# Optimization experiments

Measured on AMD Instinct MI355X. Metric: run time of the kernel, lower is better.

Reference implementation:

```python
import jax, jax.numpy as jnp
import numpy as np
from jax import lax

N_WIRES = 4
EPS_BN = 1e-5

def _conv(x, w, b):
    y = lax.conv_general_dilated(x, w, (1, 1), 'SAME',
                                 dimension_numbers=('NCHW', 'OIHW', 'NCHW'))
    return y + b[None, :, None, None]

def _bn2d(x, g, b):
    mu = jnp.mean(x, axis=(0, 2, 3), keepdims=True)
    var = jnp.var(x, axis=(0, 2, 3), keepdims=True)
    return (x - mu) * lax.rsqrt(var + EPS_BN) * g[None, :, None, None] + b[None, :, None, None]

def _maxpool2(x):
    return lax.reduce_window(x, -jnp.inf, lax.max, (1, 1, 2, 2), (1, 1, 2, 2), 'VALID')

def _ry(t):
    c, s = jnp.cos(t / 2), jnp.sin(t / 2)
    return jnp.stack([jnp.stack([c, -s], -1), jnp.stack([s, c], -1)], -2).astype(jnp.complex64)

def _rz(t):
    tc = t.astype(jnp.complex64)
    em, ep = jnp.exp(-0.5j * tc), jnp.exp(0.5j * tc)
    z = jnp.zeros_like(em)
    return jnp.stack([jnpp_stack := jnp.stack([em, z], -1), jnp.stack([z, ep], -1)], -2)

def _rx(t):
    c = jnp.cos(t / 2).astype(jnp.complex64)
    s = (-1j) * jnp.sin(t / 2).astype(jnp.complex64)
    return jnp.stack([jnp.stack([c, s], -1), jnp.stack([s, c], -1)], -2)

def _apply_1q(state, U, q):
    # state: (B,2,2,2,2); U: (2,2) shared or (B,2,2) per-sample
    a = jnp.moveaxis(state, 1 + q, 1)
    if U.ndim == 2:
        a = jnp.einsum('ij,bj...->bi...', U, a)
    else:
        a = jnp.einsum('bij,bj...->bi...', U, a)
    return jnp.moveaxis(a, 1, 1 + q)

def _cnot(state, c, t):
    a = jnp.moveaxis(state, (1 + c, 1 + t), (1, 2))
    a = jnp.stack([a[:, 0], jnp.flip(a[:, 1], axis=1)], axis=1)
    return jnp.moveaxis(a, (1, 2), (1 + c, 1 + t))

def _circuit(scaled, theta, rho):
    # scaled: (B, 4) angles; theta, rho: (4, 3)
    B = scaled.shape[0]
    state = jnp.zeros((B,) + (2,) * N_WIRES, jnp.complex64)
    state = state.at[(slice(None),) + (0,) * N_WIRES].set(1.0 + 0j)
    for i in range(N_WIRES):
        state = _apply_1q(state, _ry(scaled[:, i]), i)
    for i in range(N_WIRES):
        state = _apply_1q(state, _ry(theta[i, 0]), i)
        state = _apply_1q(state, _rz(theta[i, 1]), i)
        state = _apply_1q(state, _rx(theta[i, 2]), i)
    for i in range(N_WIRES - 1):
        state = _cnot(state, i, i + 1)
    for i in range(N_WIRES):
        state = _apply_1q(state, _ry(rho[i, 0]), i)
        state = _apply_1q(state, _rz(rho[i, 1]), i)
        state = _apply_1q(state, _rx(rho[i, 2]), i)
    for i in range(N_WIRES - 1):
        state = _cnot(state, i + 1, i)
    probs = jnp.abs(state) ** 2  # (B,2,2,2,2)
    exps = []
    for i in range(N_WIRES):
        p = jnp.moveaxis(probs, 1 + i, 1)
        exps.append(jnp.sum(p[:, 0], axis=(1, 2, 3)) - jnp.sum(p[:, 1], axis=(1, 2, 3)))
    return jnp.stack(exps, axis=1)  # (B,4)

def setup_inputs() -> dict:
    key = jax.random.key(0)
    ks = jax.random.split(key, 8)
    B = 128
    return {
        'x': jax.random.normal(ks[0], (B, 1, 224, 224), jnp.float32),
        'conv1_w': jax.random.normal(ks[1], (8, 1, 3, 3), jnp.float32) * 0.1,
        'conv1_b': jnp.zeros((8,), jnp.float32),
        'bn1_g': jnp.ones((8,), jnp.float32),
        'bn1_b': jnp.zeros((8,), jnp.float32),
        'conv2_w': jax.random.normal(ks[2], (16, 8, 3, 3), jnp.float32) * 0.1,
        'conv2_b': jnp.zeros((16,), jnp.float32),
        'bn2_g': jnp.ones((16,), jnp.float32),
        'bn2_b': jnp.zeros((16,), jnp.float32),
        'theta': jax.random.normal(ks[3], (4, 3), jnp.float32),
        'rho': jax.random.normal(ks[4], (4, 3), jnp.float32),
        'norm_g': jnp.ones((4,), jnp.float32),
        'norm_b': jnp.zeros((4,), jnp.float32),
    }

def reference(x, conv1_w, conv1_b, bn1_g, bn1_b, conv2_w, conv2_b, bn2_g, bn2_b,
              theta, rho, norm_g, norm_b):
    h = jax.nn.relu(_bn2d(_conv(x, conv1_w, conv1_b), bn1_g, bn1_b))
    h = _maxpool2(h)
    h = jax.nn.relu(_bn2d(_conv(h, conv2_w, conv2_b), bn2_g, bn2_b))
    h = _maxpool2(h)
    feat = jnp.mean(h, axis=(2, 3))          # AdaptiveAvgPool2d((1,1)) + flatten -> (B,16)
    feat = feat[:, :N_WIRES]                  # (B,4)
    scaled = (feat - jnp.mean(feat)) / (jnp.std(feat, ddof=1) + 1e-6) * jnp.pi
    out = _circuit(scaled, theta, rho)        # (B,4) real
    mu = jnp.mean(out, axis=0, keepdims=True)
    var = jnp.var(out, axis=0, keepdims=True)
    return (out - mu) * lax.rsqrt(var + EPS_BN) * norm_g[None, :] + norm_b[None, :]
```

## Files before the change

kernel.cpp:

```cpp
#include <hip/hip_runtime.h>
#include <math.h>

#define H1 224
#define W1 224
#define H2 112
#define W2 112
#define HP 56
#define WP 56

#define NS 32
#define SLOT_STRIDE 64

struct C2 { float re, im; };
__device__ __forceinline__ C2 cmul(C2 a, C2 b) {
    return C2{fmaf(a.re, b.re, -a.im * b.im), fmaf(a.re, b.im, a.im * b.re)};
}
__device__ __forceinline__ C2 cadd(C2 a, C2 b) { return C2{a.re + b.re, a.im + b.im}; }

template <int S>
__device__ __forceinline__ void ap1s(C2* st, C2 u00, C2 u01, C2 u10, C2 u11) {
#pragma unroll
    for (int i = 0; i < 16; i++) {
        if (i & S) continue;
        C2 a0 = st[i], a1 = st[i + S];
        st[i]     = cadd(cmul(u00, a0), cmul(u01, a1));
        st[i + S] = cadd(cmul(u10, a0), cmul(u11, a1));
    }
}

template <int SC, int STT>
__device__ __forceinline__ void cnot_s(C2* st) {
#pragma unroll
    for (int i = 0; i < 16; i++)
        if ((i & SC) && !(i & STT)) { C2 t = st[i]; st[i] = st[i + STT]; st[i + STT] = t; }
}

struct M2 { C2 m[2][2]; };
__device__ __forceinline__ M2 mmul(const M2& A, const M2& B) {
    M2 R;
#pragma unroll
    for (int i = 0; i < 2; i++)
#pragma unroll
        for (int j = 0; j < 2; j++)
            R.m[i][j] = cadd(cmul(A.m[i][0], B.m[0][j]), cmul(A.m[i][1], B.m[1][j]));
    return R;
}

__device__ __forceinline__ M2 combined_u(const float* __restrict__ p) {
    float c0 = cosf(0.5f * p[0]), s0 = sinf(0.5f * p[0]);
    float c1 = cosf(0.5f * p[1]), s1 = sinf(0.5f * p[1]);
    float c2 = cosf(0.5f * p[2]), s2 = sinf(0.5f * p[2]);
    M2 Ry = {{{{c0, 0.f}, {-s0, 0.f}}, {{s0, 0.f}, {c0, 0.f}}}};
    M2 Rz = {{{{c1, -s1}, {0.f, 0.f}}, {{0.f, 0.f}, {c1, s1}}}};
    M2 Rx = {{{{c2, 0.f}, {0.f, -s2}}, {{0.f, -s2}, {c2, 0.f}}}};
    return mmul(Rx, mmul(Rz, Ry));
}

template <int Q>
__device__ __forceinline__ void rows_reduce(float* red, const float* vals, int tid) {
#pragma unroll
    for (int q = 0; q < Q; q++) red[q * 256 + tid] = vals[q];
    __syncthreads();
    for (int s = 128; s > 0; s >>= 1) {
        for (int idx = tid; idx < Q * s; idx += 256) {
            int row = idx / s, i = idx - row * s;
            red[row * 256 + i] += red[row * 256 + i + s];
        }
        __syncthreads();
    }
}

__global__ void zero_ws(float* ws, int n) {
    int i = blockIdx.x * blockDim.x + threadIdx.x;
    if (i < n) ws[i] = 0.f;
}

__global__ void conv1_stats(const float* __restrict__ x, const float* __restrict__ w,
                            const float* __restrict__ bias, float* __restrict__ stats) {
    __shared__ float red[16 * 256];
    int strip = blockIdx.x;
    int b = blockIdx.y;
    int tid = threadIdx.x;
    const float* xb = x + (size_t)b * H1 * W1;
    float sums[8], sqs[8];
#pragma unroll
    for (int c = 0; c < 8; c++) { sums[c] = 0.f; sqs[c] = 0.f; }
    int col = tid;
    if (col < W1) {
        bool cl = col > 0, cr = col < W1 - 1;
        int row0 = strip * 32;
        float a0, a1, a2, b0, b1, b2, c0, c1, c2;
        {
            int r = row0 - 1;
            if (r >= 0) {
                a0 = cl ? xb[r * W1 + col - 1] : 0.f;
                a1 = xb[r * W1 + col];
                a2 = cr ? xb[r * W1 + col + 1] : 0.f;
            } else { a0 = a1 = a2 = 0.f; }
            r = row0;
            b0 = cl ? xb[r * W1 + col - 1] : 0.f;
            b1 = xb[r * W1 + col];
            b2 = cr ? xb[r * W1 + col + 1] : 0.f;
        }
        for (int rr = 0; rr < 32; rr++) {
            int rn = row0 + rr + 1;
            if (rn < H1) {
                c0 = cl ? xb[rn * W1 + col - 1] : 0.f;
                c1 = xb[rn * W1 + col];
                c2 = cr ? xb[rn * W1 + col + 1] : 0.f;
            } else { c0 = c1 = c2 = 0.f; }
#pragma unroll
            for (int c = 0; c < 8; c++) {
                float acc = bias[c];
                acc = fmaf(w[c * 9 + 0], a0, acc);
                acc = fmaf(w[c * 9 + 1], a1, acc);
                acc = fmaf(w[c * 9 + 2], a2, acc);
                acc = fmaf(w[c * 9 + 3], b0, acc);
                acc = fmaf(w[c * 9 + 4], b1, acc);
                acc = fmaf(w[c * 9 + 5], b2, acc);
                acc = fmaf(w[c * 9 + 6], c0, acc);
                acc = fmaf(w[c * 9 + 7], c1, acc);
                acc = fmaf(w[c * 9 + 8], c2, acc);
                sums[c] += acc;
                sqs[c] = fmaf(acc, acc, sqs[c]);
            }
            a0 = b0; a1 = b1; a2 = b2;
            b0 = c0; b1 = c1; b2 = c2;
        }
    }
    float vals[16];
#pragma unroll
    for (int c = 0; c < 8; c++) { vals[c] = sums[c]; vals[8 + c] = sqs[c]; }
    rows_reduce<16>(red, vals, tid);
    int slot = (b * 7 + strip) & (NS - 1);
    if (tid < 16) atomicAdd(stats + slot * SLOT_STRIDE + tid, red[tid * 256]);
}

__device__ __forceinline__ float slot_sum(const float* stats, int c) {
    float s = 0.f;
#pragma unroll
    for (int sl = 0; sl < NS; sl++) s += stats[sl * SLOT_STRIDE + c];
    return s;
}

template <int PH, int PW>
__device__ __forceinline__ void build_h1_tile(const float* __restrict__ xb,
                                              float (*h1t)[PH][PW],
                                              const float* __restrict__ w1,
                                              const float* __restrict__ b1,
                                              const float* sc1, const float* sh1,
                                              int oy0, int ox0, int tid) {
    for (int i = tid; i < PH * PW; i += 256) {
        int p = i / PW, q = i % PW;
        int hy = oy0 + p, hx = ox0 + q;
        bool ok = (hy >= 0 && hy < H2 && hx >= 0 && hx < W2);
        float xp[5][5];
        if (hy >= 1 && hy <= H2 - 2 && hx >= 1 && hx <= W2 - 2) {
            const float* bp = xb + (2 * hy - 1) * W1 + (2 * hx - 1);
#pragma unroll
            for (int r = 0; r < 5; r++)
#pragma unroll
                for (int c = 0; c < 5; c++) xp[r][c] = bp[r * W1 + c];
        } else if (ok) {
#pragma unroll
            for (int r = 0; r < 5; r++)
#pragma unroll
                for (int c = 0; c < 5; c++) {
                    int gy = 2 * hy - 1 + r, gx = 2 * hx - 1 + c;
                    xp[r][c] = (gy >= 0 && gy < H1 && gx >= 0 && gx < W1) ? xb[gy * W1 + gx] : 0.f;
                }
        }
#pragma unroll
        for (int c = 0; c < 8; c++) {
            float mx = 0.f;
            if (ok) {
                mx = -INFINITY;
#pragma unroll
                for (int dy = 0; dy < 2; dy++)
#pragma unroll
                    for (int dx = 0; dx < 2; dx++) {
                        float acc = b1[c];
#pragma unroll
                        for (int ky = 0; ky < 3; ky++)
#pragma unroll
                            for (int kx = 0; kx < 3; kx++)
                                acc = fmaf(w1[c * 9 + ky * 3 + kx], xp[dy + ky][dx + kx], acc);
                        mx = fmaxf(mx, fmaxf(fmaf(acc, sc1[c], sh1[c]), 0.f));
                    }
            }
            h1t[c][p][q] = mx;
        }
    }
}

template <bool STORE>
__global__ __launch_bounds__(256, 4) void conv2_stats_fused(
        const float* __restrict__ x, const float* __restrict__ w1,
        const float* __restrict__ b1, const float* __restrict__ g1,
        const float* __restrict__ be1, const float* __restrict__ stats1,
        const float* __restrict__ w2, const float* __restrict__ b2,
        float* __restrict__ stats2,
        float* __restrict__ pmax, float* __restrict__ pmin, float N1) {
    __shared__ __align__(16) float h1t[8][34][34];
    __shared__ float sc1[8], sh1[8];
    int b = blockIdx.z;
    int Y0 = blockIdx.y * 32, X0 = blockIdx.x * 32;
    int ty = threadIdx.y, tx = threadIdx.x;
    int tid = ty * 16 + tx;
    if (tid < 8) {
        float su = slot_sum(stats1, tid), sq = slot_sum(stats1, 8 + tid);
        float mu = su / N1;
        float var = sq / N1 - mu * mu;
        float sc = g1[tid] * rsqrtf(var + 1e-5f);
        sc1[tid] = sc;
        sh1[tid] = be1[tid] - mu * sc;
    }
    __syncthreads();
    const float* xb = x + (size_t)b * H1 * W1;
    build_h1_tile<34, 34>(xb, h1t, w1, b1, sc1, sh1, Y0 - 1, X0 - 1, tid);
    __syncthreads();
    float acc[4][2][2];
#pragma unroll
    for (int co = 0; co < 4; co++)
#pragma unroll
        for (int dy = 0; dy < 2; dy++)
#pragma unroll
            for (int dx = 0; dx < 2; dx++) acc[co][dy][dx] = b2[co];
#pragma unroll
    for (int ci = 0; ci < 8; ci++) {
        float win[4][4];
#pragma unroll
        for (int r = 0; r < 4; r++) {
            const float2* rp = (const float2*)&h1t[ci][2 * ty + r][2 * tx];
            float2 u = rp[0], v = rp[1];
            win[r][0] = u.x; win[r][1] = u.y; win[r][2] = v.x; win[r][3] = v.y;
        }
#pragma unroll
        for (int co = 0; co < 4; co++)
#pragma unroll
            for (int ky = 0; ky < 3; ky++)
#pragma unroll
                for (int kx = 0; kx < 3; kx++) {
                    float wv = w2[co * 72 + ci * 9 + ky * 3 + kx];
#pragma unroll
                    for (int dy = 0; dy < 2; dy++)
#pragma unroll
                        for (int dx = 0; dx < 2; dx++)
                            acc[co][dy][dx] = fmaf(wv, win[dy + ky][dx + kx], acc[co][dy][dx]);
                }
    }
    int cy0 = Y0 + 2 * ty, cx0 = X0 + 2 * tx;
    bool vy0 = cy0 < H2, vy1 = cy0 + 1 < H2, vx0 = cx0 < W2, vx1 = cx0 + 1 < W2;
    float vals[8];
#pragma unroll
    for (int co = 0; co < 4; co++) {
        float s = 0.f, q = 0.f;
        if (vy0 && vx0) { float a = acc[co][0][0]; s += a; q = fmaf(a, a, q); }
        if (vy0 && vx1) { float a = acc[co][0][1]; s += a; q = fmaf(a, a, q); }
        if (vy1 && vx0) { float a = acc[co][1][0]; s += a; q = fmaf(a, a, q); }
        if (vy1 && vx1) { float a = acc[co][1][1]; s += a; q = fmaf(a, a, q); }
        vals[co] = s;
        vals[4 + co] = q;
    }
    if (STORE) {
        int hy = (Y0 >> 1) + ty, hx = (X0 >> 1) + tx;
        if (hy < HP && hx < WP) {
#pragma unroll
            for (int co = 0; co < 4; co++) {
                float mx = fmaxf(fmaxf(acc[co][0][0], acc[co][0][1]),
                                 fmaxf(acc[co][1][0], acc[co][1][1]));
                float mn = fminf(fminf(acc[co][0][0], acc[co][0][1]),
                                 fminf(acc[co][1][0], acc[co][1][1]));
                size_t idx = (((size_t)b * 4 + co) * HP + hy) * WP + hx;
                pmax[idx] = mx;
                pmin[idx] = mn;
            }
        }
    }
    __syncthreads();
    float* red = (float*)h1t;
    rows_reduce<8>(red, vals, tid);
    int slot = ((b * 16) + blockIdx.y * 4 + blockIdx.x) & (NS - 1);
    if (tid < 8) atomicAdd(stats2 + slot * SLOT_STRIDE + tid, red[tid * 256]);
}

__global__ void pool_bn_mean(const float* __restrict__ pmax, const float* __restrict__ pmin,
                             const float* __restrict__ g2, const float* __restrict__ be2,
                             const float* __restrict__ stats2,
                             float* __restrict__ featbuf, float N2) {
    __shared__ float red[256];
    int co = blockIdx.x & 3;
    int b = blockIdx.x >> 2;
    int tid = threadIdx.x;
    float su = slot_sum(stats2, co), sq = slot_sum(stats2, 4 + co);
    float mu = su / N2;
    float var = sq / N2 - mu * mu;
    float sc = g2[co] * rsqrtf(var + 1e-5f);
    float sh = be2[co] - mu * sc;
    const float* P = (sc >= 0.f ? pmax : pmin) + ((size_t)b * 4 + co) * (HP * WP);
    float s = 0.f;
    for (int i = tid; i < HP * WP; i += 256) s += fmaxf(fmaf(P[i], sc, sh), 0.f);
    red[tid] = s;
    __syncthreads();
    for (int st = 128; st > 0; st >>= 1) {
        if (tid < st) red[tid] += red[tid + st];
        __syncthreads();
    }
    if (tid == 0) featbuf[(size_t)b * 4 + co] = red[0];
}

__global__ void conv2_final_fused(const float* __restrict__ x, const float* __restrict__ w1,
                                  const float* __restrict__ b1, const float* __restrict__ g1,
                                  const float* __restrict__ be1,
                                  const float* __restrict__ stats1,
                                  const float* __restrict__ w2, const float* __restrict__ b2,
                                  const float* __restrict__ g2, const float* __restrict__ be2,
                                  const float* __restrict__ stats2,
                                  float* __restrict__ featbuf, float N1, float N2) {
    __shared__ __align__(16) float h1t[8][34][34];
    __shared__ float sc1[8], sh1[8];
    __shared__ float sc2[4], sh2[4];
    int b = blockIdx.z;
    int py0 = blockIdx.y * 16, px0 = blockIdx.x * 16;
    int ty = threadIdx.y, tx = threadIdx.x;
    int tid = ty * 16 + tx;
    if (tid < 8) {
        float su = slot_sum(stats1, tid), sq = slot_sum(stats1, 8 + tid);
        float mu = su / N1;
        float var = sq / N1 - mu * mu;
        float sc = g1[tid] * rsqrtf(var + 1e-5f);
        sc1[tid] = sc;
        sh1[tid] = be1[tid] - mu * sc;
    }
    if (tid >= 16 && tid < 20) {
        int j = tid - 16;
        float su = slot_sum(stats2, j), sq = slot_sum(stats2, 4 + j);
        float mu = su / N2;
        float var = sq / N2 - mu * mu;
        float sc = g2[j] * rsqrtf(var + 1e-5f);
        sc2[j] = sc;
        sh2[j] = be2[j] - mu * sc;
    }
    __syncthreads();
    const float* xb = x + (size_t)b * H1 * W1;
    build_h1_tile<34, 34>(xb, h1t, w1, b1, sc1, sh1, 2 * py0 - 1, 2 * px0 - 1, tid);
    __syncthreads();
    bool valid = (py0 + ty < HP) && (px0 + tx < WP);
    float acc[4][2][2];
#pragma unroll
    for (int co = 0; co < 4; co++)
#pragma unroll
        for (int dy = 0; dy < 2; dy++)
#pragma unroll
            for (int dx = 0; dx < 2; dx++) acc[co][dy][dx] = b2[co];
#pragma unroll
    for (int ci = 0; ci < 8; ci++) {
        float win[4][4];
#pragma unroll
        for (int r = 0; r < 4; r++) {
            const float2* rp = (const float2*)&h1t[ci][2 * ty + r][2 * tx];
            float2 u = rp[0], v = rp[1];
            win[r][0] = u.x; win[r][1] = u.y; win[r][2] = v.x; win[r][3] = v.y;
        }
#pragma unroll
        for (int co = 0; co < 4; co++)
#pragma unroll
            for (int ky = 0; ky < 3; ky++)
#pragma unroll
                for (int kx = 0; kx < 3; kx++) {
                    float wv = w2[co * 72 + ci * 9 + ky * 3 + kx];
#pragma unroll
                    for (int dy = 0; dy < 2; dy++)
#pragma unroll
                        for (int dx = 0; dx < 2; dx++)
                            acc[co][dy][dx] = fmaf(wv, win[dy + ky][dx + kx], acc[co][dy][dx]);
                }
    }
    float vals[4];
#pragma unroll
    for (int co = 0; co < 4; co++) {
        float mx = -INFINITY;
#pragma unroll
        for (int dy = 0; dy < 2; dy++)
#pragma unroll
            for (int dx = 0; dx < 2; dx++)
                mx = fmaxf(mx, fmaxf(fmaf(acc[co][dy][dx], sc2[co], sh2[co]), 0.f));
        vals[co] = valid ? mx : 0.f;
    }
    __syncthreads();
    float* red = (float*)h1t;
    rows_reduce<4>(red, vals, tid);
    if (tid < 4) atomicAdd(featbuf + (size_t)b * 4 + tid, red[tid * 256]);
}

__device__ __forceinline__ float bsum(float v, float* lds) {
#pragma unroll
    for (int off = 32; off; off >>= 1) v += __shfl_xor(v, off, 64);
    __syncthreads();
    if ((threadIdx.x & 63) == 0) lds[threadIdx.x >> 6] = v;
    __syncthreads();
    float r = 0.f;
    int nw = (int)(blockDim.x + 63) >> 6;
#pragma clang loop unroll(disable)
    for (int i = 0; i < nw; i++) r += lds[i];
    return r;
}

__global__ void finalize(const float* __restrict__ featbuf, const float* __restrict__ theta,
                         const float* __restrict__ rho, const float* __restrict__ ng,
                         const float* __restrict__ nb, float* __restrict__ out, int B) {
    __shared__ float lds[16];
    int b = threadIdx.x;
    float f[4];
#pragma unroll
    for (int j = 0; j < 4; j++) f[j] = featbuf[b * 4 + j] * (1.f / (HP * WP));

    float n = 4.f * (float)B;
    float mean = bsum(f[0] + f[1] + f[2] + f[3], lds) / n;
    float d2 = 0.f;
#pragma unroll
    for (int j = 0; j < 4; j++) { float d = f[j] - mean; d2 += d * d; }
    float var1 = bsum(d2, lds) / (n - 1.f);
    float stdv = sqrtf(fmaxf(var1, 0.f)) + 1e-6f;
    const float PI = 3.14159265358979323846f;
    float cs[4], sn[4];
#pragma unroll
    for (int j = 0; j < 4; j++) {
        float sc = (f[j] - mean) / stdv * PI;
        cs[j] = cosf(0.5f * sc);
        sn[j] = sinf(0.5f * sc);
    }

    C2 st[16];
    {
        float amp[16];
        amp[0] = 1.f;
        amp[1] = sn[3]; amp[0] = cs[3];
#pragma unroll
        for (int k = 0; k < 2; k++) { amp[k + 2] = amp[k] * sn[2]; amp[k] *= cs[2]; }
#pragma unroll
        for (int k = 0; k < 4; k++) { amp[k + 4] = amp[k] * sn[1]; amp[k] *= cs[1]; }
#pragma unroll
        for (int k = 0; k < 8; k++) { amp[k + 8] = amp[k] * sn[0]; amp[k] *= cs[0]; }
#pragma unroll
        for (int i = 0; i < 16; i++) st[i] = C2{amp[i], 0.f};
    }

#pragma clang loop unroll(disable)
    for (int l = 0; l < 2; l++) {
        const float* p = (l == 0) ? theta : rho;
#pragma clang loop unroll(disable)
        for (int i = 0; i < 4; i++) {
            M2 U = combined_u(p + i * 3);
            switch (i) {
            case 0: ap1s<8>(st, U.m[0][0], U.m[0][1], U.m[1][0], U.m[1][1]); break;
            case 1: ap1s<4>(st, U.m[0][0], U.m[0][1], U.m[1][0], U.m[1][1]); break;
            case 2: ap1s<2>(st, U.m[0][0], U.m[0][1], U.m[1][0], U.m[1][1]); break;
            default: ap1s<1>(st, U.m[0][0], U.m[0][1], U.m[1][0], U.m[1][1]); break;
            }
        }
        if (l == 0) { cnot_s<8, 4>(st); cnot_s<4, 2>(st); cnot_s<2, 1>(st); }
        else        { cnot_s<4, 8>(st); cnot_s<2, 4>(st); cnot_s<1, 2>(st); }
    }

    float e[4];
#pragma unroll
    for (int qb = 0; qb < 4; qb++) {
        int m = 8 >> qb;
        float p0 = 0.f, p1 = 0.f;
#pragma unroll
        for (int i = 0; i < 16; i++) {
            float pr = st[i].re * st[i].re + st[i].im * st[i].im;
            if (i & m) p1 += pr; else p0 += pr;
        }
        e[qb] = p0 - p1;
    }

#pragma clang loop unroll(disable)
    for (int j = 0; j < 4; j++) {
        float mu = bsum(e[j], lds) / (float)B;
        float dv = e[j] - mu;
        float v = bsum(dv * dv, lds) / (float)B;
        out[b * 4 + j] = fmaf(dv, rsqrtf(v + 1e-5f) * ng[j], nb[j]);
    }
}

extern "C" void kernel_launch(void* const* d_in, const int* in_sizes, int n_in,
                              void* d_out, int out_size, void* d_ws, size_t ws_size,
                              hipStream_t stream) {
    const float* x     = (const float*)d_in[0];
    const float* w1    = (const float*)d_in[1];
    const float* b1    = (const float*)d_in[2];
    const float* g1    = (const float*)d_in[3];
    const float* be1   = (const float*)d_in[4];
    const float* w2    = (const float*)d_in[5];
    const float* b2    = (const float*)d_in[6];
    const float* g2    = (const float*)d_in[7];
    const float* be2   = (const float*)d_in[8];
    const float* theta = (const float*)d_in[9];
    const float* rho   = (const float*)d_in[10];
    const float* ng    = (const float*)d_in[11];
    const float* nb    = (const float*)d_in[12];
    float* out = (float*)d_out;

    int B = in_sizes[0] / (H1 * W1);

    float* ws = (float*)d_ws;
    float* stats1 = ws;
    float* stats2 = ws + NS * SLOT_STRIDE;
    float* featbuf = ws + 2 * NS * SLOT_STRIDE;
    float* pmax = featbuf + (size_t)B * 4;
    float* pmin = pmax + (size_t)B * 4 * HP * WP;

    size_t need_store = ((size_t)2 * NS * SLOT_STRIDE + (size_t)B * 4 +
                         (size_t)2 * B * 4 * HP * WP) * sizeof(float);
    bool store = ws_size >= need_store;

    float N1 = (float)B * H1 * W1;
    float N2 = (float)B * H2 * W2;
    int nz = 2 * NS * SLOT_STRIDE + B * 4;

    zero_ws<<<(nz + 255) / 256, 256, 0, stream>>>(ws, nz);
    conv1_stats<<<dim3(7, B), 256, 0, stream>>>(x, w1, b1, stats1);
    if (store) {
        conv2_stats_fused<true><<<dim3(4, 4, B), dim3(16, 16), 0, stream>>>(
            x, w1, b1, g1, be1, stats1, w2, b2, stats2, pmax, pmin, N1);
        pool_bn_mean<<<B * 4, 256, 0, stream>>>(pmax, pmin, g2, be2, stats2, featbuf, N2);
    } else {
        conv2_stats_fused<false><<<dim3(4, 4, B), dim3(16, 16), 0, stream>>>(
            x, w1, b1, g1, be1, stats1, w2, b2, stats2, nullptr, nullptr, N1);
        conv2_final_fused<<<dim3(4, 4, B), dim3(16, 16), 0, stream>>>(
            x, w1, b1, g1, be1, stats1, w2, b2, g2, be2, stats2, featbuf, N1, N2);
    }
    finalize<<<1, B, 0, stream>>>(featbuf, theta, rho, ng, nb, out, B);
}
```

Baseline: 191.6 us.

## Store pooled conv1 pre-BN output and slim conv2 to avoid recomputing conv1

Conv1 now also writes a 2x2 max- or min-pooled pre-BN map, picking max or min by the sign of the BN gamma so pooling can come before the affine BN and ReLU. Conv2 then reads this 112x112 buffer instead of recomputing conv1 from x. It stores only the sign-selected pooled value, which halves the pool2 buffer. The final stage is split into a per-sample circuit kernel plus a BN kernel that use atomic global sums, replacing the single-block finalize. This trades extra workspace traffic and more launches for removing the redundant conv1 work.

```diff
diff --git a/kernel.cpp b/kernel.cpp
--- a/kernel.cpp
+++ b/kernel.cpp
@@ -27,14 +27,12 @@
         st[i + S] = cadd(cmul(u10, a0), cmul(u11, a1));
     }
 }
-
 template <int SC, int STT>
 __device__ __forceinline__ void cnot_s(C2* st) {
 #pragma unroll
     for (int i = 0; i < 16; i++)
         if ((i & SC) && !(i & STT)) { C2 t = st[i]; st[i] = st[i + STT]; st[i + STT] = t; }
 }
-
 struct M2 { C2 m[2][2]; };
 __device__ __forceinline__ M2 mmul(const M2& A, const M2& B) {
     M2 R;
@@ -45,7 +43,6 @@
             R.m[i][j] = cadd(cmul(A.m[i][0], B.m[0][j]), cmul(A.m[i][1], B.m[1][j]));
     return R;
 }
-
 __device__ __forceinline__ M2 combined_u(const float* __restrict__ p) {
     float c0 = cosf(0.5f * p[0]), s0 = sinf(0.5f * p[0]);
     float c1 = cosf(0.5f * p[1]), s1 = sinf(0.5f * p[1]);
@@ -73,6 +70,87 @@
 __global__ void zero_ws(float* ws, int n) {
     int i = blockIdx.x * blockDim.x + threadIdx.x;
     if (i < n) ws[i] = 0.f;
+}
+
+__device__ __forceinline__ float slot_sum(const float* stats, int c) {
+    float s = 0.f;
+#pragma unroll
+    for (int sl = 0; sl < NS; sl++) s += stats[sl * SLOT_STRIDE + c];
+    return s;
+}
+
+__global__ void conv1_pool_stats(const float* __restrict__ x, const float* __restrict__ w,
+                                 const float* __restrict__ bias, const float* __restrict__ g1,
+                                 float* __restrict__ stats, float* __restrict__ p1ext) {
+    __shared__ float red[16 * 256];
+    int strip = blockIdx.x;
+    int b = blockIdx.y;
+    int tid = threadIdx.x;
+    const float* xb = x + (size_t)b * H1 * W1;
+    float sums[8], sqs[8], pm[8];
+    bool gp[8];
+#pragma unroll
+    for (int c = 0; c < 8; c++) { sums[c] = 0.f; sqs[c] = 0.f; gp[c] = g1[c] >= 0.f; }
+    int col = tid;
+    if (col < W1) {
+        bool cl = col > 0, cr = col < W1 - 1;
+        int row0 = strip * 32;
+        float a0, a1, a2, b0, b1, b2, c0, c1, c2;
+        {
+            int r = row0 - 1;
+            if (r >= 0) {
+                a0 = cl ? xb[r * W1 + col - 1] : 0.f;
+                a1 = xb[r * W1 + col];
+                a2 = cr ? xb[r * W1 + col + 1] : 0.f;
+            } else { a0 = a1 = a2 = 0.f; }
+            r = row0;
+            b0 = cl ? xb[r * W1 + col - 1] : 0.f;
+            b1 = xb[r * W1 + col];
+            b2 = cr ? xb[r * W1 + col + 1] : 0.f;
+        }
+        for (int rr = 0; rr < 32; rr++) {
+            int rn = row0 + rr + 1;
+            if (rn < H1) {
+                c0 = cl ? xb[rn * W1 + col - 1] : 0.f;
+                c1 = xb[rn * W1 + col];
+                c2 = cr ? xb[rn * W1 + col + 1] : 0.f;
+            } else { c0 = c1 = c2 = 0.f; }
+#pragma unroll
+            for (int c = 0; c < 8; c++) {
+                float acc = bias[c];
+                acc = fmaf(w[c * 9 + 0], a0, acc);
+                acc = fmaf(w[c * 9 + 1], a1, acc);
+                acc = fmaf(w[c * 9 + 2], a2, acc);
+                acc = fmaf(w[c * 9 + 3], b0, acc);
+                acc = fmaf(w[c * 9 + 4], b1, acc);
+                acc = fmaf(w[c * 9 + 5], b2, acc);
+                acc = fmaf(w[c * 9 + 6], c0, acc);
+                acc = fmaf(w[c * 9 + 7], c1, acc);
+                acc = fmaf(w[c * 9 + 8], c2, acc);
+                sums[c] += acc;
+                sqs[c] = fmaf(acc, acc, sqs[c]);
+                if ((rr & 1) == 0) {
+                    pm[c] = acc;
+                } else {
+                    float m = gp[c] ? fmaxf(pm[c], acc) : fminf(pm[c], acc);
+                    float mo = __shfl_xor(m, 1, 64);
+                    m = gp[c] ? fmaxf(m, mo) : fminf(m, mo);
+                    if ((tid & 1) == 0) {
+                        int prow = strip * 16 + (rr >> 1);
+                        p1ext[(((size_t)b * 8 + c) * H2 + prow) * W2 + (col >> 1)] = m;
+                    }
+                }
+            }
+            a0 = b0; a1 = b1; a2 = b2;
+            b0 = c0; b1 = c1; b2 = c2;
+        }
+    }
+    float vals[16];
+#pragma unroll
+    for (int c = 0; c < 8; c++) { vals[c] = sums[c]; vals[8 + c] = sqs[c]; }
+    rows_reduce<16>(red, vals, tid);
+    int slot = (b * 7 + strip) & (NS - 1);
+    if (tid < 16) atomicAdd(stats + slot * SLOT_STRIDE + tid, red[tid * 256]);
 }
 
 __global__ void conv1_stats(const float* __restrict__ x, const float* __restrict__ w,
@@ -136,13 +214,6 @@
     if (tid < 16) atomicAdd(stats + slot * SLOT_STRIDE + tid, red[tid * 256]);
 }
 
-__device__ __forceinline__ float slot_sum(const float* stats, int c) {
-    float s = 0.f;
-#pragma unroll
-    for (int sl = 0; sl < NS; sl++) s += stats[sl * SLOT_STRIDE + c];
-    return s;
-}
-
 template <int PH, int PW>
 __device__ __forceinline__ void build_h1_tile(const float* __restrict__ xb,
                                               float (*h1t)[PH][PW],
@@ -191,6 +262,99 @@
             h1t[c][p][q] = mx;
         }
     }
+}
+
+__global__ __launch_bounds__(256, 4) void conv2_stats_slim(
+        const float* __restrict__ p1ext, const float* __restrict__ g1,
+        const float* __restrict__ be1, const float* __restrict__ stats1,
+        const float* __restrict__ w2, const float* __restrict__ b2,
+        const float* __restrict__ g2,
+        float* __restrict__ stats2, float* __restrict__ p2ext, float N1) {
+    __shared__ __align__(16) float h1t[8][30][30];
+    __shared__ float sc1[8], sh1[8];
+    int b = blockIdx.z;
+    int Y0 = blockIdx.y * 28, X0 = blockIdx.x * 28;
+    int ty = threadIdx.y, tx = threadIdx.x;
+    int tid = ty * 16 + tx;
+    if (tid < 8) {
+        float su = slot_sum(stats1, tid), sq = slot_sum(stats1, 8 + tid);
+        float mu = su / N1;
+        float var = sq / N1 - mu * mu;
+        float sc = g1[tid] * rsqrtf(var + 1e-5f);
+        sc1[tid] = sc;
+        sh1[tid] = be1[tid] - mu * sc;
+    }
+    __syncthreads();
+    const float* pb = p1ext + (size_t)b * 8 * H2 * W2;
+    for (int i = tid; i < 8 * 30 * 30; i += 256) {
+        int c = i / 900, r = (i % 900) / 30, q = i % 30;
+        int hy = Y0 - 1 + r, hx = X0 - 1 + q;
+        float v = 0.f;
+        if (hy >= 0 && hy < H2 && hx >= 0 && hx < W2) {
+            float e = pb[c * H2 * W2 + hy * W2 + hx];
+            v = fmaxf(fmaf(e, sc1[c], sh1[c]), 0.f);
+        }
+        h1t[c][r][q] = v;
+    }
+    __syncthreads();
+    bool act = (ty < 14) && (tx < 14);
+    float acc[4][2][2];
+#pragma unroll
+    for (int co = 0; co < 4; co++)
+#pragma unroll
+        for (int dy = 0; dy < 2; dy++)
+#pragma unroll
+            for (int dx = 0; dx < 2; dx++) acc[co][dy][dx] = b2[co];
+    if (act) {
+#pragma unroll
+        for (int ci = 0; ci < 8; ci++) {
+            float win[4][4];
+#pragma unroll
+            for (int r = 0; r < 4; r++) {
+                const float2* rp = (const float2*)&h1t[ci][2 * ty + r][2 * tx];
+                float2 u = rp[0], v = rp[1];
+                win[r][0] = u.x; win[r][1] = u.y; win[r][2] = v.x; win[r][3] = v.y;
+            }
+#pragma unroll
+            for (int co = 0; co < 4; co++)
+#pragma unroll
+                for (int ky = 0; ky < 3; ky++)
+#pragma unroll
+                    for (int kx = 0; kx < 3; kx++) {
+                        float wv = w2[co * 72 + ci * 9 + ky * 3 + kx];
+#pragma unroll
+                        for (int dy = 0; dy < 2; dy++)
+#pragma unroll
+                            for (int dx = 0; dx < 2; dx++)
+                                acc[co][dy][dx] = fmaf(wv, win[dy + ky][dx + kx], acc[co][dy][dx]);
+                    }
+        }
+    }
+    float vals[8];
+#pragma unroll
+    for (int co = 0; co < 4; co++) {
+        float s = acc[co][0][0] + acc[co][0][1] + acc[co][1][0] + acc[co][1][1];
+        float q = acc[co][0][0] * acc[co][0][0] + acc[co][0][1] * acc[co][0][1] +
+                  acc[co][1][0] * acc[co][1][0] + acc[co][1][1] * acc[co][1][1];
+        vals[co] = act ? s : 0.f;
+        vals[4 + co] = act ? q : 0.f;
+    }
+    if (act) {
+        int hy = (Y0 >> 1) + ty, hx = (X0 >> 1) + tx;
+#pragma unroll
+        for (int co = 0; co < 4; co++) {
+            float mx = fmaxf(fmaxf(acc[co][0][0], acc[co][0][1]),
+                             fmaxf(acc[co][1][0], acc[co][1][1]));
+            float mn = fminf(fminf(acc[co][0][0], acc[co][0][1]),
+                             fminf(acc[co][1][0], acc[co][1][1]));
+            p2ext[(((size_t)b * 4 + co) * HP + hy) * WP + hx] = (g2[co] >= 0.f) ? mx : mn;
+        }
+    }
+    __syncthreads();
+    float* red = (float*)h1t;
+    rows_reduce<8>(red, vals, tid);
+    int slot = ((b * 16) + blockIdx.y * 4 + blockIdx.x) & (NS - 1);
+    if (tid < 8) atomicAdd(stats2 + slot * SLOT_STRIDE + tid, red[tid * 256]);
 }
 
 template <bool STORE>
@@ -287,7 +451,7 @@
 __global__ void pool_bn_mean(const float* __restrict__ pmax, const float* __restrict__ pmin,
                              const float* __restrict__ g2, const float* __restrict__ be2,
                              const float* __restrict__ stats2,
-                             float* __restrict__ featbuf, float N2) {
+                             float* __restrict__ featbuf, float* __restrict__ gstats, float N2) {
     __shared__ float red[256];
     int co = blockIdx.x & 3;
     int b = blockIdx.x >> 2;
@@ -306,7 +470,12 @@
         if (tid < st) red[tid] += red[tid + st];
         __syncthreads();
     }
-    if (tid == 0) featbuf[(size_t)b * 4 + co] = red[0];
+    if (tid == 0) {
+        featbuf[(size_t)b * 4 + co] = red[0];
+        float f = red[0] * (1.f / (HP * WP));
+        atomicAdd(gstats + 0, f);
+        atomicAdd(gstats + 1, f * f);
+    }
 }
 
 __global__ void conv2_final_fused(const float* __restrict__ x, const float* __restrict__ w1,
@@ -393,34 +562,16 @@
     if (tid < 4) atomicAdd(featbuf + (size_t)b * 4 + tid, red[tid * 256]);
 }
 
-__device__ __forceinline__ float bsum(float v, float* lds) {
-#pragma unroll
-    for (int off = 32; off; off >>= 1) v += __shfl_xor(v, off, 64);
-    __syncthreads();
-    if ((threadIdx.x & 63) == 0) lds[threadIdx.x >> 6] = v;
-    __syncthreads();
-    float r = 0.f;
-    int nw = (int)(blockDim.x + 63) >> 6;
-#pragma clang loop unroll(disable)
-    for (int i = 0; i < nw; i++) r += lds[i];
-    return r;
-}
-
-__global__ void finalize(const float* __restrict__ featbuf, const float* __restrict__ theta,
-                         const float* __restrict__ rho, const float* __restrict__ ng,
-                         const float* __restrict__ nb, float* __restrict__ out, int B) {
-    __shared__ float lds[16];
-    int b = threadIdx.x;
+__global__ void circuit(const float* __restrict__ featbuf, const float* __restrict__ gstats,
+                        const float* __restrict__ theta, const float* __restrict__ rho,
+                        float* __restrict__ ebuf, float* __restrict__ gst_out, int B) {
+    int b = blockIdx.x;
     float f[4];
 #pragma unroll
     for (int j = 0; j < 4; j++) f[j] = featbuf[b * 4 + j] * (1.f / (HP * WP));
-
     float n = 4.f * (float)B;
-    float mean = bsum(f[0] + f[1] + f[2] + f[3], lds) / n;
-    float d2 = 0.f;
-#pragma unroll
-    for (int j = 0; j < 4; j++) { float d = f[j] - mean; d2 += d * d; }
-    float var1 = bsum(d2, lds) / (n - 1.f);
+    float mean = gstats[0] / n;
+    float var1 = (gstats[1] - n * mean * mean) / (n - 1.f);
     float stdv = sqrtf(fmaxf(var1, 0.f)) + 1e-6f;
     const float PI = 3.14159265358979323846f;
     float cs[4], sn[4];
@@ -430,11 +581,9 @@
         cs[j] = cosf(0.5f * sc);
         sn[j] = sinf(0.5f * sc);
     }
-
     C2 st[16];
     {
         float amp[16];
-        amp[0] = 1.f;
         amp[1] = sn[3]; amp[0] = cs[3];
 #pragma unroll
         for (int k = 0; k < 2; k++) { amp[k + 2] = amp[k] * sn[2]; amp[k] *= cs[2]; }
@@ -445,7 +594,6 @@
 #pragma unroll
         for (int i = 0; i < 16; i++) st[i] = C2{amp[i], 0.f};
     }
-
 #pragma clang loop unroll(disable)
     for (int l = 0; l < 2; l++) {
         const float* p = (l == 0) ? theta : rho;
@@ -462,7 +610,102 @@
         if (l == 0) { cnot_s<8, 4>(st); cnot_s<4, 2>(st); cnot_s<2, 1>(st); }
         else        { cnot_s<4, 8>(st); cnot_s<2, 4>(st); cnot_s<1, 2>(st); }
     }
-
+    if (threadIdx.x == 0) {
+#pragma unroll
+        for (int qb = 0; qb < 4; qb++) {
+            int m = 8 >> qb;
+            float p0 = 0.f, p1 = 0.f;
+#pragma unroll
+            for (int i = 0; i < 16; i++) {
+                float pr = st[i].re * st[i].re + st[i].im * st[i].im;
+                if (i & m) p1 += pr; else p0 += pr;
+            }
+            float e = p0 - p1;
+            ebuf[(size_t)b * 4 + qb] = e;
+            atomicAdd(gst_out + 8 + qb, e);
+            atomicAdd(gst_out + 12 + qb, e * e);
+        }
+    }
+}
+
+__global__ void bn_out(const float* __restrict__ ebuf, const float* __restrict__ gstats,
+                       const float* __restrict__ ng, const float* __restrict__ nb,
+                       float* __restrict__ out, int B) {
+    int b = threadIdx.x;
+#pragma clang loop unroll(disable)
+    for (int j = 0; j < 4; j++) {
+        float mu = gstats[8 + j] / (float)B;
+        float v = gstats[12 + j] / (float)B - mu * mu;
+        float e = ebuf[(size_t)b * 4 + j];
+        out[b * 4 + j] = fmaf(e - mu, rsqrtf(fmaxf(v, 0.f) + 1e-5f) * ng[j], nb[j]);
+    }
+}
+
+__device__ __forceinline__ float bsum(float v, float* lds) {
+#pragma unroll
+    for (int off = 32; off; off >>= 1) v += __shfl_xor(v, off, 64);
+    __syncthreads();
+    if ((threadIdx.x & 63) == 0) lds[threadIdx.x >> 6] = v;
+    __syncthreads();
+    float r = 0.f;
+    int nw = (int)(blockDim.x + 63) >> 6;
+#pragma clang loop unroll(disable)
+    for (int i = 0; i < nw; i++) r += lds[i];
+    return r;
+}
+
+__global__ void finalize(const float* __restrict__ featbuf, const float* __restrict__ theta,
+                         const float* __restrict__ rho, const float* __restrict__ ng,
+                         const float* __restrict__ nb, float* __restrict__ out, int B) {
+    __shared__ float lds[16];
+    int b = threadIdx.x;
+    float f[4];
+#pragma unroll
+    for (int j = 0; j < 4; j++) f[j] = featbuf[b * 4 + j] * (1.f / (HP * WP));
+    float n = 4.f * (float)B;
+    float mean = bsum(f[0] + f[1] + f[2] + f[3], lds) / n;
+    float d2 = 0.f;
+#pragma unroll
+    for (int j = 0; j < 4; j++) { float d = f[j] - mean; d2 += d * d; }
+    float var1 = bsum(d2, lds) / (n - 1.f);
+    float stdv = sqrtf(fmaxf(var1, 0.f)) + 1e-6f;
+    const float PI = 3.14159265358979323846f;
+    float cs[4], sn[4];
+#pragma unroll
+    for (int j = 0; j < 4; j++) {
+        float sc = (f[j] - mean) / stdv * PI;
+        cs[j] = cosf(0.5f * sc);
+        sn[j] = sinf(0.5f * sc);
+    }
+    C2 st[16];
+    {
+        float amp[16];
+        amp[1] = sn[3]; amp[0] = cs[3];
+#pragma unroll
+        for (int k = 0; k < 2; k++) { amp[k + 2] = amp[k] * sn[2]; amp[k] *= cs[2]; }
+#pragma unroll
+        for (int k = 0; k < 4; k++) { amp[k + 4] = amp[k] * sn[1]; amp[k] *= cs[1]; }
+#pragma unroll
+        for (int k = 0; k < 8; k++) { amp[k + 8] = amp[k] * sn[0]; amp[k] *= cs[0]; }
+#pragma unroll
+        for (int i = 0; i < 16; i++) st[i] = C2{amp[i], 0.f};
+    }
+#pragma clang loop unroll(disable)
+    for (int l = 0; l < 2; l++) {
+        const float* p = (l == 0) ? theta : rho;
+#pragma clang loop unroll(disable)
+        for (int i = 0; i < 4; i++) {
+            M2 U = combined_u(p + i * 3);
+            switch (i) {
+            case 0: ap1s<8>(st, U.m[0][0], U.m[0][1], U.m[1][0], U.m[1][1]); break;
+            case 1: ap1s<4>(st, U.m[0][0], U.m[0][1], U.m[1][0], U.m[1][1]); break;
+            case 2: ap1s<2>(st, U.m[0][0], U.m[0][1], U.m[1][0], U.m[1][1]); break;
+            default: ap1s<1>(st, U.m[0][0], U.m[0][1], U.m[1][0], U.m[1][1]); break;
+            }
+        }
+        if (l == 0) { cnot_s<8, 4>(st); cnot_s<4, 2>(st); cnot_s<2, 1>(st); }
+        else        { cnot_s<4, 8>(st); cnot_s<2, 4>(st); cnot_s<1, 2>(st); }
+    }
     float e[4];
 #pragma unroll
     for (int qb = 0; qb < 4; qb++) {
@@ -475,7 +718,6 @@
         }
         e[qb] = p0 - p1;
     }
-
 #pragma clang loop unroll(disable)
     for (int j = 0; j < 4; j++) {
         float mu = bsum(e[j], lds) / (float)B;
@@ -508,29 +750,48 @@
     float* ws = (float*)d_ws;
     float* stats1 = ws;
     float* stats2 = ws + NS * SLOT_STRIDE;
-    float* featbuf = ws + 2 * NS * SLOT_STRIDE;
-    float* pmax = featbuf + (size_t)B * 4;
-    float* pmin = pmax + (size_t)B * 4 * HP * WP;
-
-    size_t need_store = ((size_t)2 * NS * SLOT_STRIDE + (size_t)B * 4 +
-                         (size_t)2 * B * 4 * HP * WP) * sizeof(float);
-    bool store = ws_size >= need_store;
+    float* gstats = ws + 2 * NS * SLOT_STRIDE;
+    float* featbuf = gstats + 64;
+    float* ebuf = featbuf + (size_t)B * 4;
+    float* bufs = ebuf + (size_t)B * 4;
+
+    size_t common = (size_t)(2 * NS * SLOT_STRIDE + 64) + (size_t)B * 8;
+    size_t p2n = (size_t)B * 4 * HP * WP;
+    size_t p1n = (size_t)B * 8 * H2 * W2;
+    size_t needA = (common + p2n + p1n) * sizeof(float);
+    size_t needB = (common + 2 * p2n) * sizeof(float);
+    bool tierA = ws_size >= needA;
+    bool tierB = !tierA && ws_size >= needB;
 
     float N1 = (float)B * H1 * W1;
     float N2 = (float)B * H2 * W2;
-    int nz = 2 * NS * SLOT_STRIDE + B * 4;
+    int nz = (int)common;
 
     zero_ws<<<(nz + 255) / 256, 256, 0, stream>>>(ws, nz);
-    conv1_stats<<<dim3(7, B), 256, 0, stream>>>(x, w1, b1, stats1);
-    if (store) {
+    if (tierA) {
+        float* p2ext = bufs;
+        float* p1ext = bufs + p2n;
+        conv1_pool_stats<<<dim3(7, B), 256, 0, stream>>>(x, w1, b1, g1, stats1, p1ext);
+        conv2_stats_slim<<<dim3(4, 4, B), dim3(16, 16), 0, stream>>>(
+            p1ext, g1, be1, stats1, w2, b2, g2, stats2, p2ext, N1);
+        pool_bn_mean<<<B * 4, 256, 0, stream>>>(p2ext, p2ext, g2, be2, stats2, featbuf, gstats, N2);
+        circuit<<<B, 64, 0, stream>>>(featbuf, gstats, theta, rho, ebuf, gstats, B);
+        bn_out<<<1, B, 0, stream>>>(ebuf, gstats, ng, nb, out, B);
+    } else if (tierB) {
+        float* pmax = bufs;
+        float* pmin = bufs + p2n;
+        conv1_stats<<<dim3(7, B), 256, 0, stream>>>(x, w1, b1, stats1);
         conv2_stats_fused<true><<<dim3(4, 4, B), dim3(16, 16), 0, stream>>>(
             x, w1, b1, g1, be1, stats1, w2, b2, stats2, pmax, pmin, N1);
-        pool_bn_mean<<<B * 4, 256, 0, stream>>>(pmax, pmin, g2, be2, stats2, featbuf, N2);
+        pool_bn_mean<<<B * 4, 256, 0, stream>>>(pmax, pmin, g2, be2, stats2, featbuf, gstats, N2);
+        circuit<<<B, 64, 0, stream>>>(featbuf, gstats, theta, rho, ebuf, gstats, B);
+        bn_out<<<1, B, 0, stream>>>(ebuf, gstats, ng, nb, out, B);
     } else {
+        conv1_stats<<<dim3(7, B), 256, 0, stream>>>(x, w1, b1, stats1);
         conv2_stats_fused<false><<<dim3(4, 4, B), dim3(16, 16), 0, stream>>>(
             x, w1, b1, g1, be1, stats1, w2, b2, stats2, nullptr, nullptr, N1);
         conv2_final_fused<<<dim3(4, 4, B), dim3(16, 16), 0, stream>>>(
             x, w1, b1, g1, be1, stats1, w2, b2, g2, be2, stats2, featbuf, N1, N2);
-    }
-    finalize<<<1, B, 0, stream>>>(featbuf, theta, rho, ng, nb, out, B);
-}
+        finalize<<<1, B, 0, stream>>>(featbuf, theta, rho, ng, nb, out, B);
+    }
+}
```

Measured after the change: 229.9 us. 1.2x slower.

## Split quantum finalize into per-sample circuit blocks and halve conv1 strip height

Applied to the files above, without the earlier changes.

The conv1 statistics pass now uses 16-row strips, which doubles the grid so more workgroups run at once. The single-block finalize is replaced in the stored path by three pieces. pool_bn_mean atomically accumulates the global feature sum and sum of squares. A circuit kernel then runs one block per sample and atomically accumulates the expectation statistics, and a small bn_out kernel applies the final normalization. This is meant to remove the serial single-block circuit evaluation and its block-wide reductions. In exchange it adds a launch, replaces two-pass variance with E[x²]−μ², which can lose precision, and introduces float atomics with nondeterministic summation order.

```diff
diff --git a/kernel.cpp b/kernel.cpp
--- a/kernel.cpp
+++ b/kernel.cpp
@@ -27,14 +27,12 @@
         st[i + S] = cadd(cmul(u10, a0), cmul(u11, a1));
     }
 }
-
 template <int SC, int STT>
 __device__ __forceinline__ void cnot_s(C2* st) {
 #pragma unroll
     for (int i = 0; i < 16; i++)
         if ((i & SC) && !(i & STT)) { C2 t = st[i]; st[i] = st[i + STT]; st[i + STT] = t; }
 }
-
 struct M2 { C2 m[2][2]; };
 __device__ __forceinline__ M2 mmul(const M2& A, const M2& B) {
     M2 R;
@@ -45,7 +43,6 @@
             R.m[i][j] = cadd(cmul(A.m[i][0], B.m[0][j]), cmul(A.m[i][1], B.m[1][j]));
     return R;
 }
-
 __device__ __forceinline__ M2 combined_u(const float* __restrict__ p) {
     float c0 = cosf(0.5f * p[0]), s0 = sinf(0.5f * p[0]);
     float c1 = cosf(0.5f * p[1]), s1 = sinf(0.5f * p[1]);
@@ -61,6 +58,7 @@
 #pragma unroll
     for (int q = 0; q < Q; q++) red[q * 256 + tid] = vals[q];
     __syncthreads();
+#pragma unroll
     for (int s = 128; s > 0; s >>= 1) {
         for (int idx = tid; idx < Q * s; idx += 256) {
             int row = idx / s, i = idx - row * s;
@@ -73,6 +71,13 @@
 __global__ void zero_ws(float* ws, int n) {
     int i = blockIdx.x * blockDim.x + threadIdx.x;
     if (i < n) ws[i] = 0.f;
+}
+
+__device__ __forceinline__ float slot_sum(const float* stats, int c) {
+    float s = 0.f;
+#pragma unroll
+    for (int sl = 0; sl < NS; sl++) s += stats[sl * SLOT_STRIDE + c];
+    return s;
 }
 
 __global__ void conv1_stats(const float* __restrict__ x, const float* __restrict__ w,
@@ -88,7 +93,7 @@
     int col = tid;
     if (col < W1) {
         bool cl = col > 0, cr = col < W1 - 1;
-        int row0 = strip * 32;
+        int row0 = strip * 16;
         float a0, a1, a2, b0, b1, b2, c0, c1, c2;
         {
             int r = row0 - 1;
@@ -102,7 +107,7 @@
             b1 = xb[r * W1 + col];
             b2 = cr ? xb[r * W1 + col + 1] : 0.f;
         }
-        for (int rr = 0; rr < 32; rr++) {
+        for (int rr = 0; rr < 16; rr++) {
             int rn = row0 + rr + 1;
             if (rn < H1) {
                 c0 = cl ? xb[rn * W1 + col - 1] : 0.f;
@@ -132,15 +137,8 @@
 #pragma unroll
     for (int c = 0; c < 8; c++) { vals[c] = sums[c]; vals[8 + c] = sqs[c]; }
     rows_reduce<16>(red, vals, tid);
-    int slot = (b * 7 + strip) & (NS - 1);
+    int slot = (b * 14 + strip) & (NS - 1);
     if (tid < 16) atomicAdd(stats + slot * SLOT_STRIDE + tid, red[tid * 256]);
-}
-
-__device__ __forceinline__ float slot_sum(const float* stats, int c) {
-    float s = 0.f;
-#pragma unroll
-    for (int sl = 0; sl < NS; sl++) s += stats[sl * SLOT_STRIDE + c];
-    return s;
 }
 
 template <int PH, int PW>
@@ -287,7 +285,7 @@
 __global__ void pool_bn_mean(const float* __restrict__ pmax, const float* __restrict__ pmin,
                              const float* __restrict__ g2, const float* __restrict__ be2,
                              const float* __restrict__ stats2,
-                             float* __restrict__ featbuf, float N2) {
+                             float* __restrict__ featbuf, float* __restrict__ gstats, float N2) {
     __shared__ float red[256];
     int co = blockIdx.x & 3;
     int b = blockIdx.x >> 2;
@@ -306,7 +304,12 @@
         if (tid < st) red[tid] += red[tid + st];
         __syncthreads();
     }
-    if (tid == 0) featbuf[(size_t)b * 4 + co] = red[0];
+    if (tid == 0) {
+        featbuf[(size_t)b * 4 + co] = red[0];
+        float f = red[0] * (1.f / (HP * WP));
+        atomicAdd(gstats + 0, f);
+        atomicAdd(gstats + 1, f * f);
+    }
 }
 
 __global__ void conv2_final_fused(const float* __restrict__ x, const float* __restrict__ w1,
@@ -393,34 +396,16 @@
     if (tid < 4) atomicAdd(featbuf + (size_t)b * 4 + tid, red[tid * 256]);
 }
 
-__device__ __forceinline__ float bsum(float v, float* lds) {
-#pragma unroll
-    for (int off = 32; off; off >>= 1) v += __shfl_xor(v, off, 64);
-    __syncthreads();
-    if ((threadIdx.x & 63) == 0) lds[threadIdx.x >> 6] = v;
-    __syncthreads();
-    float r = 0.f;
-    int nw = (int)(blockDim.x + 63) >> 6;
-#pragma clang loop unroll(disable)
-    for (int i = 0; i < nw; i++) r += lds[i];
-    return r;
-}
-
-__global__ void finalize(const float* __restrict__ featbuf, const float* __restrict__ theta,
-                         const float* __restrict__ rho, const float* __restrict__ ng,
-                         const float* __restrict__ nb, float* __restrict__ out, int B) {
-    __shared__ float lds[16];
-    int b = threadIdx.x;
+__global__ void circuit(const float* __restrict__ featbuf, const float* __restrict__ gstats,
+                        const float* __restrict__ theta, const float* __restrict__ rho,
+                        float* __restrict__ ebuf, float* __restrict__ gst_out, int B) {
+    int b = blockIdx.x;
     float f[4];
 #pragma unroll
     for (int j = 0; j < 4; j++) f[j] = featbuf[b * 4 + j] * (1.f / (HP * WP));
-
     float n = 4.f * (float)B;
-    float mean = bsum(f[0] + f[1] + f[2] + f[3], lds) / n;
-    float d2 = 0.f;
-#pragma unroll
-    for (int j = 0; j < 4; j++) { float d = f[j] - mean; d2 += d * d; }
-    float var1 = bsum(d2, lds) / (n - 1.f);
+    float mean = gstats[0] / n;
+    float var1 = (gstats[1] - n * mean * mean) / (n - 1.f);
     float stdv = sqrtf(fmaxf(var1, 0.f)) + 1e-6f;
     const float PI = 3.14159265358979323846f;
     float cs[4], sn[4];
@@ -430,11 +415,9 @@
         cs[j] = cosf(0.5f * sc);
         sn[j] = sinf(0.5f * sc);
     }
-
     C2 st[16];
     {
         float amp[16];
-        amp[0] = 1.f;
         amp[1] = sn[3]; amp[0] = cs[3];
 #pragma unroll
         for (int k = 0; k < 2; k++) { amp[k + 2] = amp[k] * sn[2]; amp[k] *= cs[2]; }
@@ -445,7 +428,6 @@
 #pragma unroll
         for (int i = 0; i < 16; i++) st[i] = C2{amp[i], 0.f};
     }
-
 #pragma clang loop unroll(disable)
     for (int l = 0; l < 2; l++) {
         const float* p = (l == 0) ? theta : rho;
@@ -462,7 +444,102 @@
         if (l == 0) { cnot_s<8, 4>(st); cnot_s<4, 2>(st); cnot_s<2, 1>(st); }
         else        { cnot_s<4, 8>(st); cnot_s<2, 4>(st); cnot_s<1, 2>(st); }
     }
-
+    if (threadIdx.x == 0) {
+#pragma unroll
+        for (int qb = 0; qb < 4; qb++) {
+            int m = 8 >> qb;
+            float p0 = 0.f, p1 = 0.f;
+#pragma unroll
+            for (int i = 0; i < 16; i++) {
+                float pr = st[i].re * st[i].re + st[i].im * st[i].im;
+                if (i & m) p1 += pr; else p0 += pr;
+            }
+            float e = p0 - p1;
+            ebuf[(size_t)b * 4 + qb] = e;
+            atomicAdd(gst_out + 8 + qb, e);
+            atomicAdd(gst_out + 12 + qb, e * e);
+        }
+    }
+}
+
+__global__ void bn_out(const float* __restrict__ ebuf, const float* __restrict__ gstats,
+                       const float* __restrict__ ng, const float* __restrict__ nb,
+                       float* __restrict__ out, int B) {
+    int b = threadIdx.x;
+#pragma clang loop unroll(disable)
+    for (int j = 0; j < 4; j++) {
+        float mu = gstats[8 + j] / (float)B;
+        float v = gstats[12 + j] / (float)B - mu * mu;
+        float e = ebuf[(size_t)b * 4 + j];
+        out[b * 4 + j] = fmaf(e - mu, rsqrtf(fmaxf(v, 0.f) + 1e-5f) * ng[j], nb[j]);
+    }
+}
+
+__device__ __forceinline__ float bsum(float v, float* lds) {
+#pragma unroll
+    for (int off = 32; off; off >>= 1) v += __shfl_xor(v, off, 64);
+    __syncthreads();
+    if ((threadIdx.x & 63) == 0) lds[threadIdx.x >> 6] = v;
+    __syncthreads();
+    float r = 0.f;
+    int nw = (int)(blockDim.x + 63) >> 6;
+#pragma clang loop unroll(disable)
+    for (int i = 0; i < nw; i++) r += lds[i];
+    return r;
+}
+
+__global__ void finalize(const float* __restrict__ featbuf, const float* __restrict__ theta,
+                         const float* __restrict__ rho, const float* __restrict__ ng,
+                         const float* __restrict__ nb, float* __restrict__ out, int B) {
+    __shared__ float lds[16];
+    int b = threadIdx.x;
+    float f[4];
+#pragma unroll
+    for (int j = 0; j < 4; j++) f[j] = featbuf[b * 4 + j] * (1.f / (HP * WP));
+    float n = 4.f * (float)B;
+    float mean = bsum(f[0] + f[1] + f[2] + f[3], lds) / n;
+    float d2 = 0.f;
+#pragma unroll
+    for (int j = 0; j < 4; j++) { float d = f[j] - mean; d2 += d * d; }
+    float var1 = bsum(d2, lds) / (n - 1.f);
+    float stdv = sqrtf(fmaxf(var1, 0.f)) + 1e-6f;
+    const float PI = 3.14159265358979323846f;
+    float cs[4], sn[4];
+#pragma unroll
+    for (int j = 0; j < 4; j++) {
+        float sc = (f[j] - mean) / stdv * PI;
+        cs[j] = cosf(0.5f * sc);
+        sn[j] = sinf(0.5f * sc);
+    }
+    C2 st[16];
+    {
+        float amp[16];
+        amp[1] = sn[3]; amp[0] = cs[3];
+#pragma unroll
+        for (int k = 0; k < 2; k++) { amp[k + 2] = amp[k] * sn[2]; amp[k] *= cs[2]; }
+#pragma unroll
+        for (int k = 0; k < 4; k++) { amp[k + 4] = amp[k] * sn[1]; amp[k] *= cs[1]; }
+#pragma unroll
+        for (int k = 0; k < 8; k++) { amp[k + 8] = amp[k] * sn[0]; amp[k] *= cs[0]; }
+#pragma unroll
+        for (int i = 0; i < 16; i++) st[i] = C2{amp[i], 0.f};
+    }
+#pragma clang loop unroll(disable)
+    for (int l = 0; l < 2; l++) {
+        const float* p = (l == 0) ? theta : rho;
+#pragma clang loop unroll(disable)
+        for (int i = 0; i < 4; i++) {
+            M2 U = combined_u(p + i * 3);
+            switch (i) {
+            case 0: ap1s<8>(st, U.m[0][0], U.m[0][1], U.m[1][0], U.m[1][1]); break;
+            case 1: ap1s<4>(st, U.m[0][0], U.m[0][1], U.m[1][0], U.m[1][1]); break;
+            case 2: ap1s<2>(st, U.m[0][0], U.m[0][1], U.m[1][0], U.m[1][1]); break;
+            default: ap1s<1>(st, U.m[0][0], U.m[0][1], U.m[1][0], U.m[1][1]); break;
+            }
+        }
+        if (l == 0) { cnot_s<8, 4>(st); cnot_s<4, 2>(st); cnot_s<2, 1>(st); }
+        else        { cnot_s<4, 8>(st); cnot_s<2, 4>(st); cnot_s<1, 2>(st); }
+    }
     float e[4];
 #pragma unroll
     for (int qb = 0; qb < 4; qb++) {
@@ -475,7 +552,6 @@
         }
         e[qb] = p0 - p1;
     }
-
 #pragma clang loop unroll(disable)
     for (int j = 0; j < 4; j++) {
         float mu = bsum(e[j], lds) / (float)B;
@@ -508,29 +584,35 @@
     float* ws = (float*)d_ws;
     float* stats1 = ws;
     float* stats2 = ws + NS * SLOT_STRIDE;
-    float* featbuf = ws + 2 * NS * SLOT_STRIDE;
-    float* pmax = featbuf + (size_t)B * 4;
-    float* pmin = pmax + (size_t)B * 4 * HP * WP;
-
-    size_t need_store = ((size_t)2 * NS * SLOT_STRIDE + (size_t)B * 4 +
-                         (size_t)2 * B * 4 * HP * WP) * sizeof(float);
-    bool store = ws_size >= need_store;
+    float* gstats = ws + 2 * NS * SLOT_STRIDE;
+    float* featbuf = gstats + 64;
+    float* ebuf = featbuf + (size_t)B * 4;
+    float* bufs = ebuf + (size_t)B * 4;
+
+    size_t common = (size_t)(2 * NS * SLOT_STRIDE + 64) + (size_t)B * 8;
+    size_t p2n = (size_t)B * 4 * HP * WP;
+    size_t needB = (common + 2 * p2n) * sizeof(float);
+    bool store = ws_size >= needB;
 
     float N1 = (float)B * H1 * W1;
     float N2 = (float)B * H2 * W2;
-    int nz = 2 * NS * SLOT_STRIDE + B * 4;
+    int nz = (int)common;
 
     zero_ws<<<(nz + 255) / 256, 256, 0, stream>>>(ws, nz);
-    conv1_stats<<<dim3(7, B), 256, 0, stream>>>(x, w1, b1, stats1);
+    conv1_stats<<<dim3(14, B), 256, 0, stream>>>(x, w1, b1, stats1);
     if (store) {
+        float* pmax = bufs;
+        float* pmin = bufs + p2n;
         conv2_stats_fused<true><<<dim3(4, 4, B), dim3(16, 16), 0, stream>>>(
             x, w1, b1, g1, be1, stats1, w2, b2, stats2, pmax, pmin, N1);
-        pool_bn_mean<<<B * 4, 256, 0, stream>>>(pmax, pmin, g2, be2, stats2, featbuf, N2);
+        pool_bn_mean<<<B * 4, 256, 0, stream>>>(pmax, pmin, g2, be2, stats2, featbuf, gstats, N2);
+        circuit<<<B, 64, 0, stream>>>(featbuf, gstats, theta, rho, ebuf, gstats, B);
+        bn_out<<<1, B, 0, stream>>>(ebuf, gstats, ng, nb, out, B);
     } else {
         conv2_stats_fused<false><<<dim3(4, 4, B), dim3(16, 16), 0, stream>>>(
             x, w1, b1, g1, be1, stats1, w2, b2, stats2, nullptr, nullptr, N1);
         conv2_final_fused<<<dim3(4, 4, B), dim3(16, 16), 0, stream>>>(
             x, w1, b1, g1, be1, stats1, w2, b2, g2, be2, stats2, featbuf, N1, N2);
-    }
-    finalize<<<1, B, 0, stream>>>(featbuf, theta, rho, ng, nb, out, B);
-}
+        finalize<<<1, B, 0, stream>>>(featbuf, theta, rho, ng, nb, out, B);
+    }
+}
```

After: 211.7 us. 10.5% more time.
